# Optimization experiments

Measured on AMD Instinct MI355X. Metric: run time of the kernel, lower is better.

Reference implementation:

```python
import jax, jax.numpy as jnp
import numpy as np

B, S, D = 8, 2048, 512

def setup_inputs() -> dict:
    key = jax.random.key(0)
    ks = jax.random.split(key, 9)
    scale = 1.0 / np.sqrt(D)
    q = jax.random.normal(ks[0], (B, S, D), dtype=jnp.float32)
    k = jax.random.normal(ks[1], (B, S, D), dtype=jnp.float32)
    v = jax.random.normal(ks[2], (B, S, D), dtype=jnp.float32)
    # causal mask, broadcast over batch: True = attend
    mask = jnp.tril(jnp.ones((S, S), dtype=bool))[None, :, :]
    Wq = jax.random.normal(ks[3], (D, D), dtype=jnp.float32) * scale
    bq = jax.random.normal(ks[4], (D,), dtype=jnp.float32) * scale
    Wk = jax.random.normal(ks[5], (D, D), dtype=jnp.float32) * scale
    bk = jax.random.normal(ks[6], (D,), dtype=jnp.float32) * scale
    Wv = jax.random.normal(ks[7], (D, D), dtype=jnp.float32) * scale
    bv = jax.random.normal(ks[8], (D,), dtype=jnp.float32) * scale
    return {"q": q, "k": k, "v": v, "mask": mask,
            "Wq": Wq, "bq": bq, "Wk": Wk, "bk": bk, "Wv": Wv, "bv": bv}

def reference(q, k, v, mask, Wq, bq, Wk, bk, Wv, bv):
    # torch nn.Linear: x @ W^T + b
    Q = jnp.einsum('bsd,ed->bse', q, Wq) + bq
    K = jnp.einsum('bsd,ed->bse', k, Wk) + bk
    V = jnp.einsum('bsd,ed->bse', v, Wv) + bv
    scores = jnp.einsum('bqd,bkd->bqk', Q, K) / jnp.sqrt(jnp.float32(D))
    scores = jnp.where(mask, scores, jnp.float32(-1e9))
    prob = jax.nn.softmax(scores, axis=-1)
    out = jnp.einsum('bqk,bkd->bqd', prob, V)
    return out
```

## Files before the change

### kernel.cpp

```cpp
#include <hip/hip_runtime.h>
#include <stdint.h>
#include <stddef.h>
#include <math.h>

typedef _Float16 half8 __attribute__((ext_vector_type(8)));
typedef float f32x4 __attribute__((ext_vector_type(4)));

#define SCALE_QK 0.04419417382415922f

__device__ __forceinline__ void gload16(const void* g, void* lds) {
  __builtin_amdgcn_global_load_lds(
      (const __attribute__((address_space(1))) void*)g,
      (__attribute__((address_space(3))) void*)lds,
      16, 0, 0);
}

__device__ __forceinline__ void run_kloop_wide(const float* Arow0, const _Float16* Brow0,
                                               int lda, int ldb, int kIters,
                                               _Float16* As, _Float16* Bs,
                                               f32x4 (&acc)[4][8])
{
  const int tid  = threadIdx.x;
  const int lane = tid & 63;
  const int w    = tid >> 6;
  const int wm   = w >> 1, wn = w & 1;
  const int srow = tid >> 3;
  const int sg   = tid & 7;
  const int swz  = sg ^ (srow & 7);
  const int fr   = lane & 15;
  const int fq   = lane >> 4;
  const int fx   = lane & 7;

  for (int it = 0; it < kIters; ++it) {
    const int k0 = it * 64;
    f32x4 preF[8];
    #pragma unroll
    for (int i = 0; i < 4; ++i) {
      const float* src = Arow0 + (size_t)(i*32 + srow) * lda + (k0 + sg*8);
      preF[2*i]   = *(const f32x4*)src;
      preF[2*i+1] = *(const f32x4*)(src + 4);
    }
    #pragma unroll
    for (int i = 0; i < 8; ++i)
      gload16(Brow0 + (size_t)(i*32 + srow) * ldb + (k0 + swz*8), Bs + i*2048 + w*512);
    #pragma unroll
    for (int i = 0; i < 4; ++i) {
      f32x4 x = preF[2*i], y = preF[2*i+1];
      half8 h;
      h[0]=(_Float16)x[0]; h[1]=(_Float16)x[1]; h[2]=(_Float16)x[2]; h[3]=(_Float16)x[3];
      h[4]=(_Float16)y[0]; h[5]=(_Float16)y[1]; h[6]=(_Float16)y[2]; h[7]=(_Float16)y[3];
      *(half8*)(As + (i*32 + srow)*64 + swz*8) = h;
    }
    __syncthreads();

    #pragma unroll
    for (int ks = 0; ks < 2; ++ks) {
      half8 av[4], bv[8];
      const int slot = (ks*4 + fq) ^ fx;
      #pragma unroll
      for (int i = 0; i < 4; ++i)
        av[i] = *(const half8*)(As + (wm*64 + i*16 + fr)*64 + slot*8);
      #pragma unroll
      for (int j = 0; j < 8; ++j)
        bv[j] = *(const half8*)(Bs + (wn*128 + j*16 + fr)*64 + slot*8);
      #pragma unroll
      for (int i = 0; i < 4; ++i) {
        #pragma unroll
        for (int j = 0; j < 8; ++j)
          acc[i][j] = __builtin_amdgcn_mfma_f32_16x16x32_f16(av[i], bv[j], acc[i][j], 0, 0, 0);
      }
    }
    __syncthreads();
  }
}

__device__ __forceinline__ void run_kloop_sb(const _Float16* Arow0, const _Float16* Brow0,
                                             int lda, int ldb, int kIters,
                                             _Float16* As, _Float16* Bs,
                                             f32x4 (&acc)[4][4])
{
  const int tid  = threadIdx.x;
  const int lane = tid & 63;
  const int w    = tid >> 6;
  const int wm   = w >> 1, wn = w & 1;
  const int srow = tid >> 3;
  const int sg   = tid & 7;
  const int swz  = sg ^ (srow & 7);
  const int fr   = lane & 15;
  const int fq   = lane >> 4;
  const int fx   = lane & 7;

  for (int it = 0; it < kIters; ++it) {
    const int k0 = it * 64;
    #pragma unroll
    for (int i = 0; i < 4; ++i)
      gload16(Arow0 + (size_t)(i*32 + srow) * lda + (k0 + swz*8), As + i*2048 + w*512);
    #pragma unroll
    for (int i = 0; i < 4; ++i)
      gload16(Brow0 + (size_t)(i*32 + srow) * ldb + (k0 + swz*8), Bs + i*2048 + w*512);
    __syncthreads();

    #pragma unroll
    for (int ks = 0; ks < 2; ++ks) {
      half8 av[4], bv[4];
      const int slot = (ks*4 + fq) ^ fx;
      #pragma unroll
      for (int i = 0; i < 4; ++i) {
        av[i] = *(const half8*)(As + (wm*64 + i*16 + fr)*64 + slot*8);
        bv[i] = *(const half8*)(Bs + (wn*64 + i*16 + fr)*64 + slot*8);
      }
      #pragma unroll
      for (int i = 0; i < 4; ++i) {
        #pragma unroll
        for (int j = 0; j < 4; ++j)
          acc[i][j] = __builtin_amdgcn_mfma_f32_16x16x32_f16(av[i], bv[j], acc[i][j], 0, 0, 0);
      }
    }
    __syncthreads();
  }
}

__global__ __launch_bounds__(256) void k_cvtw(const float* __restrict__ Wq,
                                              const float* __restrict__ Wk,
                                              const float* __restrict__ Wv,
                                              _Float16* __restrict__ Wb)
{
  const int t = blockIdx.x * 256 + threadIdx.x;
  const int base = t * 8;
  const int z = base >> 18;
  const int off = base & 262143;
  const float* src = (z == 0) ? Wq : ((z == 1) ? Wk : Wv);
  f32x4 a = *(const f32x4*)(src + off);
  f32x4 b = *(const f32x4*)(src + off + 4);
  half8 h;
  h[0]=(_Float16)a[0]; h[1]=(_Float16)a[1]; h[2]=(_Float16)a[2]; h[3]=(_Float16)a[3];
  h[4]=(_Float16)b[0]; h[5]=(_Float16)b[1]; h[6]=(_Float16)b[2]; h[7]=(_Float16)b[3];
  *(half8*)(Wb + base) = h;
}

__global__ __launch_bounds__(256, 2) void k_proj(const float* __restrict__ q,
                                                 const float* __restrict__ k,
                                                 const float* __restrict__ v,
                                                 const _Float16* __restrict__ Wb,
                                                 const float* __restrict__ bq,
                                                 const float* __restrict__ bk,
                                                 const float* __restrict__ bv,
                                                 _Float16* __restrict__ Qb,
                                                 _Float16* __restrict__ Kb,
                                                 _Float16* __restrict__ Vt)
{
  __shared__ __align__(16) _Float16 LDSbuf[256*132];
  _Float16* As = LDSbuf;
  _Float16* Bs = LDSbuf + 8192;

  const int bid = blockIdx.x;
  const int xcd = bid & 7, i = bid >> 3;
  const int p = xcd * 48 + (i >> 1);
  const int nt2 = i & 1;
  const int z = p >> 7, mt = p & 127;

  const float* A     = (z == 0) ? q  : (z == 1) ? k  : v;
  const float* bia   = (z == 0) ? bq : (z == 1) ? bk : bv;
  const _Float16* B  = Wb + (size_t)z * 512 * 512;

  f32x4 acc[4][8] = {};
  run_kloop_wide(A + (size_t)mt*128*512, B + (size_t)nt2*256*512, 512, 512, 8,
                 As, Bs, acc);

  const int tid = threadIdx.x;
  const int lane = tid & 63, w = tid >> 6;
  const int wm = w >> 1, wn = w & 1;
  const int fr = lane & 15, fq = lane >> 4;

  if (z < 2) {
    _Float16* C = (z == 0) ? Qb : Kb;
    const float osc = (z == 0) ? SCALE_QK : 1.0f;
    #pragma unroll
    for (int j = 0; j < 8; ++j) {
      const int col = nt2*256 + wn*128 + j*16 + fr;
      const float bval = bia[col];
      #pragma unroll
      for (int i2 = 0; i2 < 4; ++i2) {
        const int row = mt*128 + wm*64 + i2*16 + fq*4;
        #pragma unroll
        for (int r = 0; r < 4; ++r)
          C[(size_t)(row + r) * 512 + col] = (_Float16)((acc[i2][j][r] + bval) * osc);
      }
    }
  } else {
    _Float16* sm = LDSbuf;
    #pragma unroll
    for (int j = 0; j < 8; ++j) {
      const int colloc = wn*128 + j*16 + fr;
      const float bval = bia[nt2*256 + colloc];
      #pragma unroll
      for (int i2 = 0; i2 < 4; ++i2) {
        const int rowloc = wm*64 + i2*16 + fq*4;
        #pragma unroll
        for (int r = 0; r < 4; ++r)
          sm[colloc*132 + rowloc + r] = (_Float16)(acc[i2][j][r] + bval);
      }
    }
    __syncthreads();
    const int bb = mt >> 4, s0 = (mt & 15) * 128;
    #pragma unroll
    for (int q8 = 0; q8 < 16; ++q8) {
      const int dloc = q8*16 + (tid >> 4);
      const int ch   = tid & 15;
      half8 o = *(const half8*)&sm[dloc*132 + ch*8];
      *(half8*)(Vt + ((size_t)bb*512 + nt2*256 + dloc)*2048 + s0 + ch*8) = o;
    }
  }
}

__global__ __launch_bounds__(512, 4) void k_scores(const _Float16* __restrict__ Qb,
                                                   const _Float16* __restrict__ Kb,
                                                   _Float16* __restrict__ P)
{
  __shared__ __align__(16) _Float16 As[256*64], Bs[128*64];
  const int bid = blockIdx.x;
  const int b = bid & 7;
  const int t = 71 - (bid >> 3);
  int qp = 0, accum = 0;
  while (accum + 2*qp + 2 <= t) { accum += 2*qp + 2; ++qp; }
  const int kt = t - accum;
  const int qt0 = 2 * qp;

  const int tid  = threadIdx.x;
  const int lane = tid & 63;
  const int w    = tid >> 6;
  const int wm   = w >> 1, wn = w & 1;
  const int srow = tid >> 3;
  const int sg   = tid & 7;
  const int swz  = sg ^ (srow & 7);
  const int fr   = lane & 15;
  const int fq   = lane >> 4;
  const int fx   = lane & 7;

  const _Float16* Aq = Qb + ((size_t)b*2048 + (size_t)qt0*128)*512;
  const _Float16* Bk = Kb + ((size_t)b*2048 + (size_t)kt*128)*512;

  f32x4 acc[4][4] = {};
  for (int it = 0; it < 8; ++it) {
    const int k0 = it * 64;
    #pragma unroll
    for (int i = 0; i < 4; ++i)
      gload16(Aq + (size_t)(i*64 + srow) * 512 + (k0 + swz*8), As + i*4096 + w*512);
    #pragma unroll
    for (int i = 0; i < 2; ++i)
      gload16(Bk + (size_t)(i*64 + srow) * 512 + (k0 + swz*8), Bs + i*4096 + w*512);
    __syncthreads();

    #pragma unroll
    for (int ks = 0; ks < 2; ++ks) {
      half8 av[4], bv[4];
      const int slot = (ks*4 + fq) ^ fx;
      #pragma unroll
      for (int i = 0; i < 4; ++i) {
        av[i] = *(const half8*)(As + (wm*64 + i*16 + fr)*64 + slot*8);
        bv[i] = *(const half8*)(Bs + (wn*64 + i*16 + fr)*64 + slot*8);
      }
      #pragma unroll
      for (int i = 0; i < 4; ++i) {
        #pragma unroll
        for (int j = 0; j < 4; ++j)
          acc[i][j] = __builtin_amdgcn_mfma_f32_16x16x32_f16(av[i], bv[j], acc[i][j], 0, 0, 0);
      }
    }
    __syncthreads();
  }

  const int qt = qt0 + (wm >> 1);
  if (kt <= qt) {
    const bool diag = (kt == qt);
    #pragma unroll
    for (int i = 0; i < 4; ++i) {
      const int rl = (wm & 1)*64 + i*16 + fq*4;
      #pragma unroll
      for (int j = 0; j < 4; ++j) {
        const int cl = wn*64 + j*16 + fr;
        #pragma unroll
        for (int r = 0; r < 4; ++r) {
          const float sc = acc[i][j][r];
          const bool msk = diag && (cl > rl + r);
          P[((size_t)b*2048 + (size_t)qt*128 + rl + r) * 2048 + kt*128 + cl] =
              msk ? (_Float16)(-30000.0f) : (_Float16)sc;
        }
      }
    }
  }
}

__global__ __launch_bounds__(256) void k_softmax(_Float16* __restrict__ P)
{
  const int lane = threadIdx.x & 63;
  const int row  = blockIdx.x * 4 + (threadIdx.x >> 6);
  const int qIdx = row & 2047;
  _Float16* p = P + (size_t)row * 2048;
  const int L    = qIdx + 1;
  const int Lpad = ((qIdx >> 7) + 1) * 128;

  half8 xb[4];
  float m = -1e30f, s = 0.f;
  #pragma unroll
  for (int c = 0; c < 4; ++c) {
    const int i0 = lane * 8 + c * 512;
    if (i0 < Lpad) {
      half8 x = *(const half8*)(p + i0);
      xb[c] = x;
      float xv[8];
      #pragma unroll
      for (int j = 0; j < 8; ++j) xv[j] = (i0 + j < L) ? (float)x[j] : -1e30f;
      float cm = xv[0];
      #pragma unroll
      for (int j = 1; j < 8; ++j) cm = fmaxf(cm, xv[j]);
      const float mn = fmaxf(m, cm);
      float cs = 0.f;
      #pragma unroll
      for (int j = 0; j < 8; ++j) cs += __expf(xv[j] - mn);
      s = s * __expf(m - mn) + cs;
      m = mn;
    }
  }
  #pragma unroll
  for (int d = 1; d < 64; d <<= 1) {
    const float mo = __shfl_xor(m, d, 64);
    const float so = __shfl_xor(s, d, 64);
    const float mn = fmaxf(m, mo);
    s = s * __expf(m - mn) + so * __expf(mo - mn);
    m = mn;
  }
  const float inv = 1.0f / s;

  #pragma unroll
  for (int c = 0; c < 4; ++c) {
    const int i0 = lane * 8 + c * 512;
    if (i0 < Lpad) {
      half8 x = xb[c];
      half8 o;
      #pragma unroll
      for (int j = 0; j < 8; ++j)
        o[j] = (i0 + j < L) ? (_Float16)(__expf((float)x[j] - m) * inv) : (_Float16)0.f;
      *(half8*)(p + i0) = o;
    }
  }
}

__global__ __launch_bounds__(256, 4) void k_pv(const _Float16* __restrict__ P,
                                               const _Float16* __restrict__ Vt,
                                               float* __restrict__ Out)
{
  __shared__ __align__(16) _Float16 As[128*64], Bs[128*64];
  const int bid = blockIdx.x;
  const int b = bid & 7;
  const int r0 = bid >> 3;
  const int qi = r0 >> 2, dt = r0 & 3;
  const int qt = (qi & 1) ? (15 - (qi >> 1)) : (qi >> 1);

  f32x4 acc[4][4] = {};
  run_kloop_sb(P  + ((size_t)b*2048 + qt*128)*2048,
               Vt + ((size_t)b*512  + dt*128)*2048,
               2048, 2048, (qt + 1) * 2, As, Bs, acc);
  const int lane = threadIdx.x & 63, w = threadIdx.x >> 6;
  const int wm = w >> 1, wn = w & 1;
  const int fr = lane & 15, fq = lane >> 4;
  #pragma unroll
  for (int i = 0; i < 4; ++i) {
    const int row = qt*128 + wm*64 + i*16 + fq*4;
    #pragma unroll
    for (int j = 0; j < 4; ++j) {
      const int col = dt*128 + wn*64 + j*16 + fr;
      #pragma unroll
      for (int r = 0; r < 4; ++r)
        Out[((size_t)b*2048 + row + r) * 512 + col] = acc[i][j][r];
    }
  }
}

extern "C" void kernel_launch(void* const* d_in, const int* in_sizes, int n_in,
                              void* d_out, int out_size, void* d_ws, size_t ws_size,
                              hipStream_t stream) {
  (void)in_sizes; (void)n_in; (void)out_size;
  const float* q  = (const float*)d_in[0];
  const float* k  = (const float*)d_in[1];
  const float* v  = (const float*)d_in[2];
  const float* Wq = (const float*)d_in[4];
  const float* bq = (const float*)d_in[5];
  const float* Wk = (const float*)d_in[6];
  const float* bk = (const float*)d_in[7];
  const float* Wv = (const float*)d_in[8];
  const float* bv = (const float*)d_in[9];

  const size_t OFF_P  = 0;
  const size_t OFF_Q  = (size_t)64 << 20;
  const size_t OFF_K  = (size_t)80 << 20;
  const size_t OFF_VT = (size_t)112 << 20;
  const size_t OFF_W  = (size_t)128 << 20;
  const size_t NEEDED = OFF_W + (size_t)3 * 512 * 512 * sizeof(_Float16);
  if (ws_size < NEEDED) return;

  char* ws = (char*)d_ws;
  _Float16* P  = (_Float16*)(ws + OFF_P);
  _Float16* Qb = (_Float16*)(ws + OFF_Q);
  _Float16* Kb = (_Float16*)(ws + OFF_K);
  _Float16* Vt = (_Float16*)(ws + OFF_VT);
  _Float16* Wb = (_Float16*)(ws + OFF_W);
  float* Out = (float*)d_out;

  k_cvtw   <<<dim3(384),  dim3(256), 0, stream>>>(Wq, Wk, Wv, Wb);
  k_proj   <<<dim3(768),  dim3(256), 0, stream>>>(q, k, v, Wb, bq, bk, bv, Qb, Kb, Vt);
  k_scores <<<dim3(576),  dim3(512), 0, stream>>>(Qb, Kb, P);
  k_softmax<<<dim3(4096), dim3(256), 0, stream>>>(P);
  k_pv     <<<dim3(512),  dim3(256), 0, stream>>>(P, Vt, Out);
}
```

Baseline: 266.3 us.

## Shrink proj LDS for higher occupancy and split PV into narrower tiles

k_proj's shared buffer shrinks from 256x132 to 24576 halves. The V-transpose epilogue now writes two 128-column halves in sequence through the smaller buffer, which lets launch bounds rise to 3 blocks per CU. k_pv now uses 128x64 output tiles with an inlined k-loop, which doubles the grid to 1024 blocks. A new static q-tile map interleaves long and short causal rows for load balance. This buys occupancy and parallelism at the cost of more syncs in k_proj and rereading the P tiles twice as often in k_pv.

```diff
diff --git a/kernel.cpp b/kernel.cpp
--- a/kernel.cpp
+++ b/kernel.cpp
@@ -67,52 +67,6 @@
       for (int i = 0; i < 4; ++i) {
         #pragma unroll
         for (int j = 0; j < 8; ++j)
-          acc[i][j] = __builtin_amdgcn_mfma_f32_16x16x32_f16(av[i], bv[j], acc[i][j], 0, 0, 0);
-      }
-    }
-    __syncthreads();
-  }
-}
-
-__device__ __forceinline__ void run_kloop_sb(const _Float16* Arow0, const _Float16* Brow0,
-                                             int lda, int ldb, int kIters,
-                                             _Float16* As, _Float16* Bs,
-                                             f32x4 (&acc)[4][4])
-{
-  const int tid  = threadIdx.x;
-  const int lane = tid & 63;
-  const int w    = tid >> 6;
-  const int wm   = w >> 1, wn = w & 1;
-  const int srow = tid >> 3;
-  const int sg   = tid & 7;
-  const int swz  = sg ^ (srow & 7);
-  const int fr   = lane & 15;
-  const int fq   = lane >> 4;
-  const int fx   = lane & 7;
-
-  for (int it = 0; it < kIters; ++it) {
-    const int k0 = it * 64;
-    #pragma unroll
-    for (int i = 0; i < 4; ++i)
-      gload16(Arow0 + (size_t)(i*32 + srow) * lda + (k0 + swz*8), As + i*2048 + w*512);
-    #pragma unroll
-    for (int i = 0; i < 4; ++i)
-      gload16(Brow0 + (size_t)(i*32 + srow) * ldb + (k0 + swz*8), Bs + i*2048 + w*512);
-    __syncthreads();
-
-    #pragma unroll
-    for (int ks = 0; ks < 2; ++ks) {
-      half8 av[4], bv[4];
-      const int slot = (ks*4 + fq) ^ fx;
-      #pragma unroll
-      for (int i = 0; i < 4; ++i) {
-        av[i] = *(const half8*)(As + (wm*64 + i*16 + fr)*64 + slot*8);
-        bv[i] = *(const half8*)(Bs + (wn*64 + i*16 + fr)*64 + slot*8);
-      }
-      #pragma unroll
-      for (int i = 0; i < 4; ++i) {
-        #pragma unroll
-        for (int j = 0; j < 4; ++j)
           acc[i][j] = __builtin_amdgcn_mfma_f32_16x16x32_f16(av[i], bv[j], acc[i][j], 0, 0, 0);
       }
     }
@@ -138,7 +92,7 @@
   *(half8*)(Wb + base) = h;
 }
 
-__global__ __launch_bounds__(256, 2) void k_proj(const float* __restrict__ q,
+__global__ __launch_bounds__(256, 3) void k_proj(const float* __restrict__ q,
                                                  const float* __restrict__ k,
                                                  const float* __restrict__ v,
                                                  const _Float16* __restrict__ Wb,
@@ -149,7 +103,7 @@
                                                  _Float16* __restrict__ Kb,
                                                  _Float16* __restrict__ Vt)
 {
-  __shared__ __align__(16) _Float16 LDSbuf[256*132];
+  __shared__ __align__(16) _Float16 LDSbuf[24576];
   _Float16* As = LDSbuf;
   _Float16* Bs = LDSbuf + 8192;
 
@@ -189,26 +143,32 @@
     }
   } else {
     _Float16* sm = LDSbuf;
-    #pragma unroll
-    for (int j = 0; j < 8; ++j) {
-      const int colloc = wn*128 + j*16 + fr;
-      const float bval = bia[nt2*256 + colloc];
-      #pragma unroll
-      for (int i2 = 0; i2 < 4; ++i2) {
-        const int rowloc = wm*64 + i2*16 + fq*4;
-        #pragma unroll
-        for (int r = 0; r < 4; ++r)
-          sm[colloc*132 + rowloc + r] = (_Float16)(acc[i2][j][r] + bval);
-      }
-    }
-    __syncthreads();
     const int bb = mt >> 4, s0 = (mt & 15) * 128;
     #pragma unroll
-    for (int q8 = 0; q8 < 16; ++q8) {
-      const int dloc = q8*16 + (tid >> 4);
-      const int ch   = tid & 15;
-      half8 o = *(const half8*)&sm[dloc*132 + ch*8];
-      *(half8*)(Vt + ((size_t)bb*512 + nt2*256 + dloc)*2048 + s0 + ch*8) = o;
+    for (int h = 0; h < 2; ++h) {
+      if (wn == h) {
+        #pragma unroll
+        for (int j = 0; j < 8; ++j) {
+          const int dl = j*16 + fr;
+          const float bval = bia[nt2*256 + h*128 + dl];
+          #pragma unroll
+          for (int i2 = 0; i2 < 4; ++i2) {
+            const int rowloc = wm*64 + i2*16 + fq*4;
+            #pragma unroll
+            for (int r = 0; r < 4; ++r)
+              sm[dl*132 + rowloc + r] = (_Float16)(acc[i2][j][r] + bval);
+          }
+        }
+      }
+      __syncthreads();
+      #pragma unroll
+      for (int q8 = 0; q8 < 8; ++q8) {
+        const int dloc = q8*16 + (tid >> 4);
+        const int ch   = tid & 15;
+        half8 o = *(const half8*)&sm[dloc*132 + ch*8];
+        *(half8*)(Vt + ((size_t)bb*512 + nt2*256 + h*128 + dloc)*2048 + s0 + ch*8) = o;
+      }
+      if (h == 0) __syncthreads();
     }
   }
 }
@@ -350,26 +310,66 @@
                                                const _Float16* __restrict__ Vt,
                                                float* __restrict__ Out)
 {
-  __shared__ __align__(16) _Float16 As[128*64], Bs[128*64];
+  __shared__ __align__(16) _Float16 As[128*64], Bs[64*64];
+  static const int QTMAP[16] = {15,13,11,9, 0,2,4,6, 14,12,10,8, 1,3,5,7};
   const int bid = blockIdx.x;
   const int b = bid & 7;
   const int r0 = bid >> 3;
-  const int qi = r0 >> 2, dt = r0 & 3;
-  const int qt = (qi & 1) ? (15 - (qi >> 1)) : (qi >> 1);
-
-  f32x4 acc[4][4] = {};
-  run_kloop_sb(P  + ((size_t)b*2048 + qt*128)*2048,
-               Vt + ((size_t)b*512  + dt*128)*2048,
-               2048, 2048, (qt + 1) * 2, As, Bs, acc);
-  const int lane = threadIdx.x & 63, w = threadIdx.x >> 6;
-  const int wm = w >> 1, wn = w & 1;
-  const int fr = lane & 15, fq = lane >> 4;
+  const int qi = r0 >> 3, dt = r0 & 7;
+  const int qt = QTMAP[qi];
+  const int kIters = (qt + 1) * 2;
+
+  const int tid  = threadIdx.x;
+  const int lane = tid & 63;
+  const int w    = tid >> 6;
+  const int wm   = w >> 1, wn = w & 1;
+  const int srow = tid >> 3;
+  const int sg   = tid & 7;
+  const int swz  = sg ^ (srow & 7);
+  const int fr   = lane & 15;
+  const int fq   = lane >> 4;
+  const int fx   = lane & 7;
+
+  const _Float16* Ap = P  + ((size_t)b*2048 + qt*128)*2048;
+  const _Float16* Bv = Vt + ((size_t)b*512  + dt*64)*2048;
+
+  f32x4 acc[4][2] = {};
+  for (int it = 0; it < kIters; ++it) {
+    const int k0 = it * 64;
+    #pragma unroll
+    for (int i = 0; i < 4; ++i)
+      gload16(Ap + (size_t)(i*32 + srow) * 2048 + (k0 + swz*8), As + i*2048 + w*512);
+    #pragma unroll
+    for (int i = 0; i < 2; ++i)
+      gload16(Bv + (size_t)(i*32 + srow) * 2048 + (k0 + swz*8), Bs + i*2048 + w*512);
+    __syncthreads();
+
+    #pragma unroll
+    for (int ks = 0; ks < 2; ++ks) {
+      half8 av[4], bv[2];
+      const int slot = (ks*4 + fq) ^ fx;
+      #pragma unroll
+      for (int i = 0; i < 4; ++i)
+        av[i] = *(const half8*)(As + (wm*64 + i*16 + fr)*64 + slot*8);
+      #pragma unroll
+      for (int j = 0; j < 2; ++j)
+        bv[j] = *(const half8*)(Bs + (wn*32 + j*16 + fr)*64 + slot*8);
+      #pragma unroll
+      for (int i = 0; i < 4; ++i) {
+        #pragma unroll
+        for (int j = 0; j < 2; ++j)
+          acc[i][j] = __builtin_amdgcn_mfma_f32_16x16x32_f16(av[i], bv[j], acc[i][j], 0, 0, 0);
+      }
+    }
+    __syncthreads();
+  }
+
   #pragma unroll
   for (int i = 0; i < 4; ++i) {
     const int row = qt*128 + wm*64 + i*16 + fq*4;
     #pragma unroll
-    for (int j = 0; j < 4; ++j) {
-      const int col = dt*128 + wn*64 + j*16 + fr;
+    for (int j = 0; j < 2; ++j) {
+      const int col = dt*64 + wn*32 + j*16 + fr;
       #pragma unroll
       for (int r = 0; r < 4; ++r)
         Out[((size_t)b*2048 + row + r) * 512 + col] = acc[i][j][r];
@@ -411,5 +411,5 @@
   k_proj   <<<dim3(768),  dim3(256), 0, stream>>>(q, k, v, Wb, bq, bk, bv, Qb, Kb, Vt);
   k_scores <<<dim3(576),  dim3(512), 0, stream>>>(Qb, Kb, P);
   k_softmax<<<dim3(4096), dim3(256), 0, stream>>>(P);
-  k_pv     <<<dim3(512),  dim3(256), 0, stream>>>(P, Vt, Out);
-}
+  k_pv     <<<dim3(1024), dim3(256), 0, stream>>>(P, Vt, Out);
+}
```

New measurement: 292.1 us. 9.7% more time.
